# Optimization experiments

Hardware: AMD Instinct MI355X
Metric: run time of the kernel (lower is better)

The kernel has to match this reference:

```python
import jax, jax.numpy as jnp
import numpy as np

N = 10000    # nodes
D = 128      # d_model
K = 16       # d_state
S = 5        # seq_len (tokens per node)
E = 320000   # edges
R = 200      # num relation types
P = E // (S - 1)  # edges sampled per tokenizer step
EPS = 1e-5


def setup_inputs() -> dict:
    key = jax.random.key(0)
    ks = jax.random.split(key, 16)
    sc = 1.0 / np.sqrt(D)
    return {
        "x": jax.random.normal(ks[0], (N, D), jnp.float32),
        "edge_index": jax.random.randint(ks[1], (2, E), 0, N),
        "edge_type": jax.random.randint(ks[2], (E,), 0, R),
        "perms": jax.random.randint(ks[3], (S - 1, P), 0, E),
        "rel_table": jax.random.normal(ks[4], (R, D), jnp.float32) * 0.1,
        "log_A": jax.random.normal(ks[5], (D, K), jnp.float32) * 0.1,
        "W_B": jax.random.normal(ks[6], (D, K), jnp.float32) * sc,
        "W_C": jax.random.normal(ks[7], (D, K), jnp.float32) * sc,
        "W_delta": jax.random.normal(ks[8], (D, D), jnp.float32) * sc,
        "b_delta": jnp.zeros((D,), jnp.float32),
        "W_g": jax.random.normal(ks[9], (D, D), jnp.float32) * sc,
        "b_g": jnp.zeros((D,), jnp.float32),
        "W_out": jax.random.normal(ks[10], (D, D), jnp.float32) * sc,
        "b_out": jnp.zeros((D,), jnp.float32),
        "ln_g": jnp.ones((D,), jnp.float32),
        "ln_b": jnp.zeros((D,), jnp.float32),
    }


def _tokenize(x, edge_index, edge_type, perms, rel_table):
    # x: [N,D]; perms: [S-1,P] -> tokens [N,S,D]
    src, dst = edge_index[0], edge_index[1]
    step_src = src[perms]                    # [S-1,P]
    step_dst = dst[perms]                    # [S-1,P]
    msg = x[step_src] + rel_table[edge_type[perms]]  # [S-1,P,D]
    seg = jax.vmap(lambda i, m: jax.ops.segment_sum(m, i, num_segments=N))(step_dst, msg)  # [S-1,N,D]
    deg = jax.vmap(lambda i: jax.ops.segment_sum(jnp.ones((P,), x.dtype), i, num_segments=N))(step_dst)  # [S-1,N]
    neigh = seg / jnp.clip(deg, 1.0)[..., None]
    return jnp.concatenate([x[:, None, :], jnp.moveaxis(neigh, 0, 1)], axis=1)  # [N,S,D]


def _selective_scan(tokens, log_A, W_B, W_C, W_delta, b_delta):
    # tokens: [N,S,D] -> [N,S,D]
    deltas = jax.nn.softplus(tokens @ W_delta + b_delta)  # [N,S,D]
    Bs = tokens @ W_B                                     # [N,S,K]
    Cs = tokens @ W_C                                     # [N,S,K]
    A_cont = -jnp.exp(log_A)                              # [D,K]
    A_disc = jnp.exp(deltas[..., None] * A_cont)          # [N,S,D,K]
    Bx = deltas[..., None] * Bs[:, :, None, :] * tokens[..., None]  # [N,S,D,K] = B_disc * x_k

    def step(state, xs):
        a, bx, c = xs                          # [N,D,K],[N,D,K],[N,K]
        state = a * state + bx
        y = jnp.einsum('ndk,nk->nd', state, c)
        return state, y

    init = jnp.zeros((tokens.shape[0], D, K), tokens.dtype)
    _, ys = jax.lax.scan(step, init, (jnp.moveaxis(A_disc, 1, 0),
                                      jnp.moveaxis(Bx, 1, 0),
                                      jnp.moveaxis(Cs, 1, 0)))
    return jnp.moveaxis(ys, 0, 1)  # [N,S,D]


def reference(x, edge_index, edge_type, perms, rel_table, log_A, W_B, W_C,
              W_delta, b_delta, W_g, b_g, W_out, b_out, ln_g, ln_b):
    tokens = _tokenize(x, edge_index, edge_type, perms, rel_table)
    out_f = _selective_scan(tokens, log_A, W_B, W_C, W_delta, b_delta)
    out_b = _selective_scan(tokens[:, ::-1, :], log_A, W_B, W_C, W_delta, b_delta)
    scan_out = (out_f + out_b[:, ::-1, :]).mean(axis=1)  # [N,D]
    gate = jax.nn.silu(x @ W_g + b_g)
    res = x + gate * (scan_out @ W_out + b_out)
    mu = res.mean(axis=-1, keepdims=True)
    var = res.var(axis=-1, keepdims=True)
    return (res - mu) / jnp.sqrt(var + EPS) * ln_g + ln_b
```

## Files before the change

kernel.cpp:

```cpp
#include <hip/hip_runtime.h>
#include <hip/hip_bf16.h>
#include <math.h>

#define N_NODES 10000
#define D_MODEL 128
#define E_EDGES 320000
#define P_EDGES 80000
#define LN_EPS 1e-5f
#define NBUCK 40960
#define CAP 32
#define M_ROWS 50000
#define M_PAD  50048
#define NPAD   320

typedef __attribute__((ext_vector_type(8))) short bf16x8;
typedef __attribute__((ext_vector_type(4))) float f32x4;

__device__ __forceinline__ unsigned short f2bf(float f) {
    __hip_bfloat16 h = __float2bfloat16(f);
    return *reinterpret_cast<unsigned short*>(&h);
}
__device__ __forceinline__ float bf2f(unsigned int u) {
    return __uint_as_float(u << 16);
}

__global__ __launch_bounds__(256) void prep_all(
    const float* __restrict__ Wd, const float* __restrict__ Wb,
    const float* __restrict__ Wc, const float* __restrict__ Wg,
    const float* __restrict__ W_out,
    const float* __restrict__ x, const float* __restrict__ rel,
    const int* __restrict__ edge_index, const int* __restrict__ edge_type,
    unsigned short* __restrict__ Bp, unsigned short* __restrict__ Wop,
    unsigned short* __restrict__ x_bf, unsigned short* __restrict__ rel_bf,
    int* __restrict__ cnt, int4* __restrict__ ed4,
    unsigned short* __restrict__ tokens)
{
    int gid = blockIdx.x * 256 + threadIdx.x;
    if (gid < 40960) {
        int k = gid / NPAD, n = gid - (gid / NPAD) * NPAD;
        float v = 0.f;
        if (n < 128)      v = Wd[k * 128 + n];
        else if (n < 144) v = Wb[k * 16 + (n - 128)];
        else if (n < 160) v = Wc[k * 16 + (n - 144)];
        else if (n < 288) v = Wg[k * 128 + (n - 160)];
        Bp[((size_t)(k >> 3) * NPAD + n) * 8 + (k & 7)] = f2bf(v);
    } else if (gid < 57344) {
        int i = gid - 40960;
        int k = i >> 7, n = i & 127;
        Wop[((size_t)(k >> 3) * 128 + n) * 8 + (k & 7)] = f2bf(W_out[k * 128 + n]);
    } else if (gid < 98304) {
        cnt[gid - 57344] = 0;
    } else if (gid < 123904) {
        int i = gid - 98304;
        rel_bf[i] = f2bf(rel[i]);
    } else if (gid < 1403904) {
        int i = gid - 123904;
        unsigned short v = f2bf(x[i]);
        x_bf[i] = v;
        tokens[(size_t)(i >> 7) * 640 + (i & 127)] = v;
    } else if (gid < 1723904) {
        int e = gid - 1403904;
        ed4[e] = make_int4(edge_index[e], edge_index[E_EDGES + e], edge_type[e], 0);
    }
}

__global__ __launch_bounds__(256) void csr_build(
    const int4* __restrict__ ed4, const int* __restrict__ perms,
    int* __restrict__ cnt, int2* __restrict__ slots)
{
    int gid = blockIdx.x * blockDim.x + threadIdx.x;
    if (gid >= 4 * P_EDGES) return;
    int s = gid / P_EDGES;
    int e = perms[gid];
    int4 ed = ed4[e];
    int b = ed.y * 4 + s;
    int pos = atomicAdd(&cnt[b], 1);
    if (pos < CAP) slots[(size_t)b * CAP + pos] = make_int2(ed.x, ed.z);
}

__global__ __launch_bounds__(256) void gather_tokens(
    const unsigned short* __restrict__ x_bf,
    const int* __restrict__ cnt, const int2* __restrict__ slots,
    const unsigned short* __restrict__ rel_bf,
    unsigned short* __restrict__ tokens)
{
    int n = blockIdx.x;
    int w = threadIdx.x >> 6, lane = threadIdx.x & 63;
    int b = n * 4 + w;
    int c = cnt[b];
    int cc = c < CAP ? c : CAP;
    const int2* sl = slots + (size_t)b * CAP;
    const unsigned int* xu = (const unsigned int*)x_bf;
    const unsigned int* ru = (const unsigned int*)rel_bf;
    float ax = 0.f, ay = 0.f;
    int j = 0;
    for (; j + 4 <= cc; j += 4) {
        int4 e01 = *(const int4*)(sl + j);
        int4 e23 = *(const int4*)(sl + j + 2);
        unsigned int x0 = xu[(size_t)e01.x * 64 + lane];
        unsigned int r0 = ru[(size_t)e01.y * 64 + lane];
        unsigned int x1 = xu[(size_t)e01.z * 64 + lane];
        unsigned int r1 = ru[(size_t)e01.w * 64 + lane];
        unsigned int x2 = xu[(size_t)e23.x * 64 + lane];
        unsigned int r2 = ru[(size_t)e23.y * 64 + lane];
        unsigned int x3 = xu[(size_t)e23.z * 64 + lane];
        unsigned int r3 = ru[(size_t)e23.w * 64 + lane];
        ax += (bf2f(x0 & 0xffffu) + bf2f(r0 & 0xffffu))
            + (bf2f(x1 & 0xffffu) + bf2f(r1 & 0xffffu))
            + (bf2f(x2 & 0xffffu) + bf2f(r2 & 0xffffu))
            + (bf2f(x3 & 0xffffu) + bf2f(r3 & 0xffffu));
        ay += (bf2f(x0 >> 16) + bf2f(r0 >> 16))
            + (bf2f(x1 >> 16) + bf2f(r1 >> 16))
            + (bf2f(x2 >> 16) + bf2f(r2 >> 16))
            + (bf2f(x3 >> 16) + bf2f(r3 >> 16));
    }
    if (j + 2 <= cc) {
        int4 e01 = *(const int4*)(sl + j);
        unsigned int x0 = xu[(size_t)e01.x * 64 + lane];
        unsigned int r0 = ru[(size_t)e01.y * 64 + lane];
        unsigned int x1 = xu[(size_t)e01.z * 64 + lane];
        unsigned int r1 = ru[(size_t)e01.w * 64 + lane];
        ax += (bf2f(x0 & 0xffffu) + bf2f(r0 & 0xffffu))
            + (bf2f(x1 & 0xffffu) + bf2f(r1 & 0xffffu));
        ay += (bf2f(x0 >> 16) + bf2f(r0 >> 16))
            + (bf2f(x1 >> 16) + bf2f(r1 >> 16));
        j += 2;
    }
    if (j < cc) {
        int2 se = sl[j];
        unsigned int xa = xu[(size_t)se.x * 64 + lane];
        unsigned int ra = ru[(size_t)se.y * 64 + lane];
        ax += bf2f(xa & 0xffffu) + bf2f(ra & 0xffffu);
        ay += bf2f(xa >> 16) + bf2f(ra >> 16);
    }
    float inv = 1.f / fmaxf((float)c, 1.f);
    unsigned int pack = (unsigned int)f2bf(ax * inv)
                      | ((unsigned int)f2bf(ay * inv) << 16);
    ((unsigned int*)tokens)[((size_t)n * 5 + w + 1) * 64 + lane] = pack;
}

__global__ __launch_bounds__(256) void mfma_gemm(
    const unsigned short* __restrict__ tokens,
    const unsigned short* __restrict__ Bp,
    const float* __restrict__ b_delta, const float* __restrict__ b_g,
    unsigned short* __restrict__ delta,
    unsigned short* __restrict__ bc,
    unsigned short* __restrict__ g)
{
    int m0 = blockIdx.x * 64, n0 = blockIdx.y * 64;
    int wv = threadIdx.x >> 6, lane = threadIdx.x & 63;
    int quad = lane >> 4, l16 = lane & 15;

    f32x4 acc[4] = {{0,0,0,0},{0,0,0,0},{0,0,0,0},{0,0,0,0}};
    const unsigned short* arow = tokens + (size_t)(m0 + wv * 16 + l16) * 128 + quad * 8;
    #pragma unroll
    for (int kc = 0; kc < 128; kc += 32) {
        bf16x8 a = *(const bf16x8*)(arow + kc);
        #pragma unroll
        for (int t = 0; t < 4; ++t) {
            bf16x8 b = *(const bf16x8*)(Bp + ((size_t)(kc / 8 + quad) * NPAD + n0 + 16 * t + l16) * 8);
            acc[t] = __builtin_amdgcn_mfma_f32_16x16x32_bf16(a, b, acc[t], 0, 0, 0);
        }
    }

    int rbase = m0 + wv * 16 + quad * 4;
    #pragma unroll
    for (int t = 0; t < 4; ++t) {
        int c = n0 + 16 * t + l16;
        #pragma unroll
        for (int reg = 0; reg < 4; ++reg) {
            int r = rbase + reg;
            if (r >= M_ROWS) continue;
            float v = acc[t][reg];
            if (c < 128) {
                float z = v + b_delta[c];
                float d = (z > 15.f) ? z : log1pf(__expf(z));
                delta[(size_t)r * 128 + c] = f2bf(d);
            } else if (c < 160) {
                bc[(size_t)r * 32 + (c - 128)] = f2bf(v);
            } else if (c < 288) {
                int rq = r / 5;
                if (r - rq * 5 == 0)
                    g[(size_t)rq * 128 + (c - 160)] = f2bf(v + b_g[c - 160]);
            }
        }
    }
}

__global__ __launch_bounds__(128) void scan_so(
    const unsigned short* __restrict__ tokens,
    const unsigned short* __restrict__ delta,
    const unsigned short* __restrict__ bcbuf,
    const float* __restrict__ log_A,
    unsigned short* __restrict__ so)
{
    const int n = blockIdx.x, t = threadIdx.x;
    __shared__ __align__(16) float BC[160];

    for (int idx = t; idx < 160; idx += 128)
        BC[idx] = bf2f(bcbuf[(size_t)n * 160 + idx]);

    float tv[5], dl[5];
    {
        const unsigned short* tb = tokens + (size_t)n * 640 + t;
        const unsigned short* db = delta  + (size_t)n * 640 + t;
        #pragma unroll
        for (int s = 0; s < 5; ++s) {
            tv[s] = bf2f(tb[s * 128]);
            dl[s] = bf2f(db[s * 128]);
        }
    }
    float Ac[16];
    {
        const float4* la = (const float4*)(log_A + t * 16);
        #pragma unroll
        for (int q = 0; q < 4; ++q) {
            float4 lv = la[q];
            Ac[q * 4 + 0] = -__expf(lv.x);
            Ac[q * 4 + 1] = -__expf(lv.y);
            Ac[q * 4 + 2] = -__expf(lv.z);
            Ac[q * 4 + 3] = -__expf(lv.w);
        }
    }
    __syncthreads();

    float st[16], V[16];
    #pragma unroll
    for (int k = 0; k < 16; ++k) { st[k] = 0.f; V[k] = BC[16 + k]; }
    float total = 0.f;
    #pragma unroll
    for (int s = 0; s < 5; ++s) {
        float dtv = dl[s] * tv[s];
        float yf = 0.f, ub = 0.f;
        #pragma unroll
        for (int k = 0; k < 16; ++k) {
            float B = BC[s * 32 + k];
            float C = BC[s * 32 + 16 + k];
            float A = __expf(dl[s] * Ac[k]);
            st[k] = fmaf(A, st[k], dtv * B);
            yf = fmaf(st[k], C, yf);
            ub = fmaf(V[k], B, ub);
            if (s < 4) V[k] = fmaf(A, V[k], BC[(s + 1) * 32 + 16 + k]);
        }
        total += yf + dtv * ub;
    }
    so[(size_t)n * 128 + t] = f2bf(total * 0.2f);
}

__global__ __launch_bounds__(256) void out_gemm(
    const unsigned short* __restrict__ so,
    const unsigned short* __restrict__ Wop,
    const unsigned short* __restrict__ gbuf,
    const float* __restrict__ x,
    const float* __restrict__ b_out,
    const float* __restrict__ ln_g, const float* __restrict__ ln_b,
    float* __restrict__ out)
{
    int m0 = blockIdx.x * 16;
    int tid = threadIdx.x;
    int wv = tid >> 6, lane = tid & 63;
    int quad = lane >> 4, l16 = lane & 15;

    __shared__ float res[16 * 132];
    __shared__ float pmu[16][16];
    __shared__ float pv2[16][16];
    __shared__ float muA[16], rstdA[16];

    f32x4 acc[2] = {{0,0,0,0},{0,0,0,0}};
    const unsigned short* arow = so + (size_t)(m0 + l16) * 128 + quad * 8;
    #pragma unroll
    for (int kc = 0; kc < 128; kc += 32) {
        bf16x8 a = *(const bf16x8*)(arow + kc);
        #pragma unroll
        for (int tt = 0; tt < 2; ++tt) {
            int t = wv * 2 + tt;
            bf16x8 b = *(const bf16x8*)(Wop + ((size_t)(kc / 8 + quad) * 128 + 16 * t + l16) * 8);
            acc[tt] = __builtin_amdgcn_mfma_f32_16x16x32_bf16(a, b, acc[tt], 0, 0, 0);
        }
    }

    #pragma unroll
    for (int tt = 0; tt < 2; ++tt) {
        int c = wv * 32 + tt * 16 + l16;
        #pragma unroll
        for (int reg = 0; reg < 4; ++reg) {
            int lrow = quad * 4 + reg;
            int r = m0 + lrow;
            float o = acc[tt][reg] + b_out[c];
            float gl = bf2f(gbuf[(size_t)r * 128 + c]);
            float gate = gl / (1.f + __expf(-gl));
            res[lrow * 132 + c] = x[(size_t)r * 128 + c] + gate * o;
        }
    }
    __syncthreads();

    {
        int row = tid >> 4, q = tid & 15;
        float s = 0.f, s2 = 0.f;
        #pragma unroll
        for (int i = 0; i < 8; ++i) {
            float v = res[row * 132 + q + 16 * i];
            s += v; s2 += v * v;
        }
        pmu[row][q] = s; pv2[row][q] = s2;
    }
    __syncthreads();
    if (tid < 16) {
        float s = 0.f, s2 = 0.f;
        #pragma unroll
        for (int i = 0; i < 16; ++i) { s += pmu[tid][i]; s2 += pv2[tid][i]; }
        float mu = s * (1.f / 128.f);
        float var = s2 * (1.f / 128.f) - mu * mu;
        muA[tid] = mu;
        rstdA[tid] = rsqrtf(var + LN_EPS);
    }
    __syncthreads();
    #pragma unroll
    for (int i = 0; i < 8; ++i) {
        int idx = i * 256 + tid;
        int row = idx >> 7, c = idx & 127;
        out[(size_t)(m0 + row) * 128 + c] =
            (res[row * 132 + c] - muA[row]) * rstdA[row] * ln_g[c] + ln_b[c];
    }
}

extern "C" void kernel_launch(void* const* d_in, const int* in_sizes, int n_in,
                              void* d_out, int out_size, void* d_ws, size_t ws_size,
                              hipStream_t stream) {
    const float* x          = (const float*)d_in[0];
    const int*   edge_index = (const int*)  d_in[1];
    const int*   edge_type  = (const int*)  d_in[2];
    const int*   perms      = (const int*)  d_in[3];
    const float* rel_table  = (const float*)d_in[4];
    const float* log_A      = (const float*)d_in[5];
    const float* W_B        = (const float*)d_in[6];
    const float* W_C        = (const float*)d_in[7];
    const float* W_delta    = (const float*)d_in[8];
    const float* b_delta    = (const float*)d_in[9];
    const float* W_g        = (const float*)d_in[10];
    const float* b_g        = (const float*)d_in[11];
    const float* W_out      = (const float*)d_in[12];
    const float* b_out      = (const float*)d_in[13];
    const float* ln_g       = (const float*)d_in[14];
    const float* ln_b       = (const float*)d_in[15];

    char* ws = (char*)d_ws;
    int*            cnt    = (int*)           (ws + 0);
    unsigned short* Bp     = (unsigned short*)(ws + 163840);
    unsigned short* Wop    = (unsigned short*)(ws + 245760);
    unsigned short* x_bf   = (unsigned short*)(ws + 278528);
    unsigned short* rel_bf = (unsigned short*)(ws + 2838528);
    int4*           ed4    = (int4*)          (ws + 2889728);
    unsigned short* tokens = (unsigned short*)(ws + 8009728);
    unsigned short* g      = (unsigned short*)(ws + 20822016);
    unsigned short* bc     = (unsigned short*)(ws + 23382016);
    int2*           slots  = (int2*)          (ws + 26582016);
    unsigned short* delta  = (unsigned short*)(ws + 26582016);
    unsigned short* so     = (unsigned short*)(ws + 39394304);

    prep_all<<<(1723904 + 255) / 256, 256, 0, stream>>>(
        W_delta, W_B, W_C, W_g, W_out, x, rel_table, edge_index, edge_type,
        Bp, Wop, x_bf, rel_bf, cnt, ed4, tokens);

    csr_build<<<(4 * P_EDGES + 255) / 256, 256, 0, stream>>>(
        ed4, perms, cnt, slots);

    gather_tokens<<<N_NODES, 256, 0, stream>>>(
        x_bf, cnt, slots, rel_bf, tokens);

    mfma_gemm<<<dim3(M_PAD / 64, NPAD / 64), 256, 0, stream>>>(
        tokens, Bp, b_delta, b_g, delta, bc, g);

    scan_so<<<N_NODES, 128, 0, stream>>>(
        tokens, delta, bc, log_A, so);

    out_gemm<<<N_NODES / 16, 256, 0, stream>>>(
        so, Wop, g, x, b_out, ln_g, ln_b, (float*)d_out);
}
```

Baseline: 198.9 us.

## Move gate GEMM into output kernel and drop padded columns from token GEMM

The gate projection x@W_g used to be computed for every token row (5x redundant, keeping only s=0 rows) inside the big token GEMM. It now runs as a second MFMA inside out_gemm, using x_bf and a packed Wgp. The token GEMM shrinks from 320 padded columns over a 2D grid to 160 columns, with each block computing all of them across 10 accumulators. This removes redundant MFMA work and the g buffer round trip through memory, but raises register pressure in mfma_gemm and adds loads to out_gemm.

```diff
diff --git a/kernel.cpp b/kernel.cpp
--- a/kernel.cpp
+++ b/kernel.cpp
@@ -11,7 +11,7 @@
 #define CAP 32
 #define M_ROWS 50000
 #define M_PAD  50048
-#define NPAD   320
+#define NCOLS 160
 
 typedef __attribute__((ext_vector_type(8))) short bf16x8;
 typedef __attribute__((ext_vector_type(4))) float f32x4;
@@ -31,35 +31,39 @@
     const float* __restrict__ x, const float* __restrict__ rel,
     const int* __restrict__ edge_index, const int* __restrict__ edge_type,
     unsigned short* __restrict__ Bp, unsigned short* __restrict__ Wop,
+    unsigned short* __restrict__ Wgp,
     unsigned short* __restrict__ x_bf, unsigned short* __restrict__ rel_bf,
     int* __restrict__ cnt, int4* __restrict__ ed4,
     unsigned short* __restrict__ tokens)
 {
     int gid = blockIdx.x * 256 + threadIdx.x;
-    if (gid < 40960) {
-        int k = gid / NPAD, n = gid - (gid / NPAD) * NPAD;
-        float v = 0.f;
+    if (gid < 20480) {
+        int k = gid / NCOLS, n = gid - (gid / NCOLS) * NCOLS;
+        float v;
         if (n < 128)      v = Wd[k * 128 + n];
         else if (n < 144) v = Wb[k * 16 + (n - 128)];
-        else if (n < 160) v = Wc[k * 16 + (n - 144)];
-        else if (n < 288) v = Wg[k * 128 + (n - 160)];
-        Bp[((size_t)(k >> 3) * NPAD + n) * 8 + (k & 7)] = f2bf(v);
-    } else if (gid < 57344) {
-        int i = gid - 40960;
+        else              v = Wc[k * 16 + (n - 144)];
+        Bp[((size_t)(k >> 3) * NCOLS + n) * 8 + (k & 7)] = f2bf(v);
+    } else if (gid < 36864) {
+        int i = gid - 20480;
         int k = i >> 7, n = i & 127;
         Wop[((size_t)(k >> 3) * 128 + n) * 8 + (k & 7)] = f2bf(W_out[k * 128 + n]);
-    } else if (gid < 98304) {
-        cnt[gid - 57344] = 0;
-    } else if (gid < 123904) {
-        int i = gid - 98304;
+    } else if (gid < 53248) {
+        int i = gid - 36864;
+        int k = i >> 7, n = i & 127;
+        Wgp[((size_t)(k >> 3) * 128 + n) * 8 + (k & 7)] = f2bf(Wg[k * 128 + n]);
+    } else if (gid < 94208) {
+        cnt[gid - 53248] = 0;
+    } else if (gid < 119808) {
+        int i = gid - 94208;
         rel_bf[i] = f2bf(rel[i]);
-    } else if (gid < 1403904) {
-        int i = gid - 123904;
+    } else if (gid < 1399808) {
+        int i = gid - 119808;
         unsigned short v = f2bf(x[i]);
         x_bf[i] = v;
         tokens[(size_t)(i >> 7) * 640 + (i & 127)] = v;
-    } else if (gid < 1723904) {
-        int e = gid - 1403904;
+    } else if (gid < 1719808) {
+        int e = gid - 1399808;
         ed4[e] = make_int4(edge_index[e], edge_index[E_EDGES + e], edge_type[e], 0);
     }
 }
@@ -142,46 +146,44 @@
 __global__ __launch_bounds__(256) void mfma_gemm(
     const unsigned short* __restrict__ tokens,
     const unsigned short* __restrict__ Bp,
-    const float* __restrict__ b_delta, const float* __restrict__ b_g,
+    const float* __restrict__ b_delta,
     unsigned short* __restrict__ delta,
-    unsigned short* __restrict__ bc,
-    unsigned short* __restrict__ g)
-{
-    int m0 = blockIdx.x * 64, n0 = blockIdx.y * 64;
+    unsigned short* __restrict__ bc)
+{
+    int m0 = blockIdx.x * 64;
     int wv = threadIdx.x >> 6, lane = threadIdx.x & 63;
     int quad = lane >> 4, l16 = lane & 15;
 
-    f32x4 acc[4] = {{0,0,0,0},{0,0,0,0},{0,0,0,0},{0,0,0,0}};
+    f32x4 acc[10];
+    #pragma unroll
+    for (int t = 0; t < 10; ++t) acc[t] = (f32x4){0.f, 0.f, 0.f, 0.f};
+
     const unsigned short* arow = tokens + (size_t)(m0 + wv * 16 + l16) * 128 + quad * 8;
     #pragma unroll
     for (int kc = 0; kc < 128; kc += 32) {
         bf16x8 a = *(const bf16x8*)(arow + kc);
         #pragma unroll
-        for (int t = 0; t < 4; ++t) {
-            bf16x8 b = *(const bf16x8*)(Bp + ((size_t)(kc / 8 + quad) * NPAD + n0 + 16 * t + l16) * 8);
+        for (int t = 0; t < 10; ++t) {
+            bf16x8 b = *(const bf16x8*)(Bp + ((size_t)(kc / 8 + quad) * NCOLS + 16 * t + l16) * 8);
             acc[t] = __builtin_amdgcn_mfma_f32_16x16x32_bf16(a, b, acc[t], 0, 0, 0);
         }
     }
 
     int rbase = m0 + wv * 16 + quad * 4;
     #pragma unroll
-    for (int t = 0; t < 4; ++t) {
-        int c = n0 + 16 * t + l16;
+    for (int t = 0; t < 10; ++t) {
+        int c = 16 * t + l16;
         #pragma unroll
         for (int reg = 0; reg < 4; ++reg) {
             int r = rbase + reg;
             if (r >= M_ROWS) continue;
             float v = acc[t][reg];
-            if (c < 128) {
+            if (t < 8) {
                 float z = v + b_delta[c];
                 float d = (z > 15.f) ? z : log1pf(__expf(z));
                 delta[(size_t)r * 128 + c] = f2bf(d);
-            } else if (c < 160) {
+            } else {
                 bc[(size_t)r * 32 + (c - 128)] = f2bf(v);
-            } else if (c < 288) {
-                int rq = r / 5;
-                if (r - rq * 5 == 0)
-                    g[(size_t)rq * 128 + (c - 160)] = f2bf(v + b_g[c - 160]);
             }
         }
     }
@@ -250,9 +252,10 @@
 __global__ __launch_bounds__(256) void out_gemm(
     const unsigned short* __restrict__ so,
     const unsigned short* __restrict__ Wop,
-    const unsigned short* __restrict__ gbuf,
+    const unsigned short* __restrict__ Wgp,
+    const unsigned short* __restrict__ x_bf,
     const float* __restrict__ x,
-    const float* __restrict__ b_out,
+    const float* __restrict__ b_out, const float* __restrict__ b_g,
     const float* __restrict__ ln_g, const float* __restrict__ ln_b,
     float* __restrict__ out)
 {
@@ -266,16 +269,22 @@
     __shared__ float pv2[16][16];
     __shared__ float muA[16], rstdA[16];
 
-    f32x4 acc[2] = {{0,0,0,0},{0,0,0,0}};
-    const unsigned short* arow = so + (size_t)(m0 + l16) * 128 + quad * 8;
+    f32x4 accO[2] = {{0,0,0,0},{0,0,0,0}};
+    f32x4 accG[2] = {{0,0,0,0},{0,0,0,0}};
+    const unsigned short* arow = so   + (size_t)(m0 + l16) * 128 + quad * 8;
+    const unsigned short* grow = x_bf + (size_t)(m0 + l16) * 128 + quad * 8;
     #pragma unroll
     for (int kc = 0; kc < 128; kc += 32) {
-        bf16x8 a = *(const bf16x8*)(arow + kc);
+        bf16x8 a  = *(const bf16x8*)(arow + kc);
+        bf16x8 ag = *(const bf16x8*)(grow + kc);
         #pragma unroll
         for (int tt = 0; tt < 2; ++tt) {
             int t = wv * 2 + tt;
-            bf16x8 b = *(const bf16x8*)(Wop + ((size_t)(kc / 8 + quad) * 128 + 16 * t + l16) * 8);
-            acc[tt] = __builtin_amdgcn_mfma_f32_16x16x32_bf16(a, b, acc[tt], 0, 0, 0);
+            size_t bi = ((size_t)(kc / 8 + quad) * 128 + 16 * t + l16) * 8;
+            bf16x8 bo = *(const bf16x8*)(Wop + bi);
+            bf16x8 bg = *(const bf16x8*)(Wgp + bi);
+            accO[tt] = __builtin_amdgcn_mfma_f32_16x16x32_bf16(a,  bo, accO[tt], 0, 0, 0);
+            accG[tt] = __builtin_amdgcn_mfma_f32_16x16x32_bf16(ag, bg, accG[tt], 0, 0, 0);
         }
     }
 
@@ -286,8 +295,8 @@
         for (int reg = 0; reg < 4; ++reg) {
             int lrow = quad * 4 + reg;
             int r = m0 + lrow;
-            float o = acc[tt][reg] + b_out[c];
-            float gl = bf2f(gbuf[(size_t)r * 128 + c]);
+            float o  = accO[tt][reg] + b_out[c];
+            float gl = accG[tt][reg] + b_g[c];
             float gate = gl / (1.f + __expf(-gl));
             res[lrow * 132 + c] = x[(size_t)r * 128 + c] + gate * o;
         }
@@ -347,20 +356,20 @@
     char* ws = (char*)d_ws;
     int*            cnt    = (int*)           (ws + 0);
     unsigned short* Bp     = (unsigned short*)(ws + 163840);
-    unsigned short* Wop    = (unsigned short*)(ws + 245760);
-    unsigned short* x_bf   = (unsigned short*)(ws + 278528);
-    unsigned short* rel_bf = (unsigned short*)(ws + 2838528);
-    int4*           ed4    = (int4*)          (ws + 2889728);
-    unsigned short* tokens = (unsigned short*)(ws + 8009728);
-    unsigned short* g      = (unsigned short*)(ws + 20822016);
-    unsigned short* bc     = (unsigned short*)(ws + 23382016);
-    int2*           slots  = (int2*)          (ws + 26582016);
-    unsigned short* delta  = (unsigned short*)(ws + 26582016);
-    unsigned short* so     = (unsigned short*)(ws + 39394304);
-
-    prep_all<<<(1723904 + 255) / 256, 256, 0, stream>>>(
+    unsigned short* Wop    = (unsigned short*)(ws + 204800);
+    unsigned short* Wgp    = (unsigned short*)(ws + 237568);
+    unsigned short* x_bf   = (unsigned short*)(ws + 270336);
+    unsigned short* rel_bf = (unsigned short*)(ws + 2830336);
+    int4*           ed4    = (int4*)          (ws + 2881536);
+    unsigned short* tokens = (unsigned short*)(ws + 8001536);
+    unsigned short* bc     = (unsigned short*)(ws + 20813824);
+    int2*           slots  = (int2*)          (ws + 24013824);
+    unsigned short* delta  = (unsigned short*)(ws + 24013824);
+    unsigned short* so     = (unsigned short*)(ws + 36826112);
+
+    prep_all<<<6718, 256, 0, stream>>>(
         W_delta, W_B, W_C, W_g, W_out, x, rel_table, edge_index, edge_type,
-        Bp, Wop, x_bf, rel_bf, cnt, ed4, tokens);
+        Bp, Wop, Wgp, x_bf, rel_bf, cnt, ed4, tokens);
 
     csr_build<<<(4 * P_EDGES + 255) / 256, 256, 0, stream>>>(
         ed4, perms, cnt, slots);
@@ -368,12 +377,12 @@
     gather_tokens<<<N_NODES, 256, 0, stream>>>(
         x_bf, cnt, slots, rel_bf, tokens);
 
-    mfma_gemm<<<dim3(M_PAD / 64, NPAD / 64), 256, 0, stream>>>(
-        tokens, Bp, b_delta, b_g, delta, bc, g);
+    mfma_gemm<<<M_PAD / 64, 256, 0, stream>>>(
+        tokens, Bp, b_delta, delta, bc);
 
     scan_so<<<N_NODES, 128, 0, stream>>>(
         tokens, delta, bc, log_A, so);
 
     out_gemm<<<N_NODES / 16, 256, 0, stream>>>(
-        so, Wop, g, x, b_out, ln_g, ln_b, (float*)d_out);
-}
+        so, Wop, Wgp, x_bf, x, b_out, b_g, ln_g, ln_b, (float*)d_out);
+}
```

New measurement: 206.6 us. 3.9% more time.
